# Kernel optimization log

Measured on AMD Instinct MI355X. Metric: run time of the kernel, lower is better.

## Reference

```python
import jax, jax.numpy as jnp
import numpy as np


def setup_inputs() -> dict:
    key = jax.random.key(0)
    k1, k2, k3 = jax.random.split(key, 3)
    N, C_in, H, W = 32, 16, 256, 256
    C_out, K = 64, 3
    x = jax.random.normal(k1, (N, C_in, H, W), dtype=jnp.float32)
    # match nn.Conv2d default init scale roughly (values irrelevant for correctness harness)
    fan_in = C_in * K * K
    bound = 1.0 / np.sqrt(fan_in)
    conv_weight = jax.random.normal(k2, (C_out, C_in, K, K), dtype=jnp.float32) * bound
    conv_bias = jax.random.normal(k3, (C_out,), dtype=jnp.float32) * bound
    return {"x": x, "conv_weight": conv_weight, "conv_bias": conv_bias}


def reference(x, conv_weight, conv_bias):
    # Conv2d: stride=1, padding=0 (VALID), dilation=1, groups=1
    y = jax.lax.conv_general_dilated(
        x, conv_weight,
        window_strides=(1, 1), padding='VALID',
        dimension_numbers=('NCHW', 'OIHW', 'NCHW'),
    ) + conv_bias[None, :, None, None]          # (N, C_out, OH, OW)
    y = jnp.min(y, axis=1, keepdims=True)       # min over output channels -> (N, 1, OH, OW)
    return jnp.tanh(jnp.tanh(y))                # double tanh
```

## Files before the change

### kernel.cpp

```cpp
#include <hip/hip_runtime.h>
#include <hip/hip_bf16.h>

typedef __attribute__((ext_vector_type(8)))  short short8;
typedef __attribute__((ext_vector_type(4)))  float f32x4;
typedef __attribute__((ext_vector_type(16))) float f32x16;

#define CIN   16
#define HH    256
#define WW    256
#define OHH   254
#define OWW   254
#define HW    (HH * WW)

#define SLOTU  (36 * 8)
#define HALF_R (16 * SLOTU + 8)

__device__ __forceinline__ ushort f2bf(float f) {
    unsigned u = __builtin_bit_cast(unsigned, f);
    unsigned r = (u + 0x7fffu + ((u >> 16) & 1u)) >> 16;
    return (ushort)r;
}

__device__ __forceinline__ float dtanh2(float x) {
    const float K = 2.8853900817779268f;
    float xc = fminf(fmaxf(x, -9.0f), 9.0f);
    float e1 = __builtin_amdgcn_exp2f(K * xc);
    float t1 = 1.0f - 2.0f * __builtin_amdgcn_rcpf(e1 + 1.0f);
    float e2 = __builtin_amdgcn_exp2f(K * t1);
    return 1.0f - 2.0f * __builtin_amdgcn_rcpf(e2 + 1.0f);
}

__global__ void prep_weights(const float* __restrict__ wsrc, ushort* __restrict__ wfrag) {
    int idx = blockIdx.x * 256 + threadIdx.x;
    if (idx >= 9216) return;
    int r    = idx & 7;
    int lane = (idx >> 3) & 63;
    int j    = (idx >> 9) & 1;
    int tap  = idx >> 10;
    int ci   = 8 * (lane >> 5) + r;
    int co   = j * 32 + (lane & 31);
    int kh   = tap / 3, kw = tap - 3 * kh;
    wfrag[idx] = f2bf(wsrc[(co * CIN + ci) * 9 + kh * 3 + kw]);
}

__global__ __launch_bounds__(256, 2) void conv_min_tanh(
        const float* __restrict__ x, const ushort* __restrict__ wfrag,
        const float* __restrict__ bias, float* __restrict__ out) {
    __shared__ ushort ring[2 * HALF_R];
    __shared__ ushort mp[2][2][4][32];

    const int tid   = threadIdx.x;
    const int ow0   = blockIdx.x * 32;
    const int hbase = blockIdx.y * 128;
    const int n     = blockIdx.z;
    const float* xb = x + (size_t)n * CIN * HW;

    auto stage_inline = [&](int pos) {
        int lr  = pos / 36;
        int rm  = pos - lr * 36;
        int ciq = rm / 9;
        int w4  = rm - ciq * 9;
        int hg  = min(hbase + lr, HH - 1);
        int wg  = min(ow0 + 4 * w4, WW - 4);
        const float* src = xb + (size_t)(ciq * 4) * HW + hg * WW + wg;
        f32x4 v0 = *reinterpret_cast<const f32x4*>(src);
        f32x4 v1 = *reinterpret_cast<const f32x4*>(src + HW);
        f32x4 v2 = *reinterpret_cast<const f32x4*>(src + 2 * HW);
        f32x4 v3 = *reinterpret_cast<const f32x4*>(src + 3 * HW);
        ushort* dst = &ring[(ciq >> 1) * HALF_R + lr * SLOTU + (4 * w4) * 8 + (ciq & 1) * 4];
#pragma unroll
        for (int e = 0; e < 4; ++e) {
            unsigned lo, hi;
            asm("v_cvt_pk_bf16_f32 %0, %1, %2" : "=v"(lo) : "v"(v0[e]), "v"(v1[e]));
            asm("v_cvt_pk_bf16_f32 %0, %1, %2" : "=v"(hi) : "v"(v2[e]), "v"(v3[e]));
            uint2 pk; pk.x = lo; pk.y = hi;
            *reinterpret_cast<uint2*>(dst + e * 8) = pk;
        }
    };
    stage_inline(tid);
    if (tid < 32) stage_inline(tid + 256);

    const bool sa = (tid < 144);
    const int lr  = tid / 36;
    const int rm  = tid - lr * 36;
    const int ciq = rm / 9;
    const int w4  = rm - ciq * 9;
    const int wg  = min(ow0 + 4 * w4, WW - 4);
    const float* gbase = xb + (size_t)(ciq * 4) * HW + wg;
    ushort* sdst = &ring[(ciq >> 1) * HALF_R + (4 * w4) * 8 + (ciq & 1) * 4];

    f32x4 ra0 = {}, ra1 = {}, ra2 = {}, ra3 = {};
    f32x4 rb0 = {}, rb1 = {}, rb2 = {}, rb3 = {};

#define ISSUE(cc, r0, r1, r2, r3)                                              \
    if (sa) {                                                                  \
        int hg = min(hbase + 4 * (cc) + lr, HH - 1);                           \
        const float* s_ = gbase + hg * WW;                                     \
        asm volatile("global_load_dwordx4 %0, %1, off" : "=v"(r0) : "v"(s_) : "memory");           \
        asm volatile("global_load_dwordx4 %0, %1, off" : "=v"(r1) : "v"(s_ + HW) : "memory");      \
        asm volatile("global_load_dwordx4 %0, %1, off" : "=v"(r2) : "v"(s_ + 2 * HW) : "memory");  \
        asm volatile("global_load_dwordx4 %0, %1, off" : "=v"(r3) : "v"(s_ + 3 * HW) : "memory");  \
    }

#define WRITEBK(cc, r0, r1, r2, r3)                                            \
    if (sa) {                                                                  \
        ushort* d_ = sdst + ((4 * (cc) + lr) & 15) * SLOTU;                    \
        _Pragma("unroll")                                                      \
        for (int e = 0; e < 4; ++e) {                                          \
            unsigned lo_, hi_;                                                 \
            asm("v_cvt_pk_bf16_f32 %0, %1, %2" : "=v"(lo_) : "v"(r0[e]), "v"(r1[e]));  \
            asm("v_cvt_pk_bf16_f32 %0, %1, %2" : "=v"(hi_) : "v"(r2[e]), "v"(r3[e]));  \
            uint2 pk_; pk_.x = lo_; pk_.y = hi_;                               \
            *reinterpret_cast<uint2*>(d_ + e * 8) = pk_;                       \
        }                                                                      \
    }

    ISSUE(2, ra0, ra1, ra2, ra3);
    ISSUE(3, rb0, rb1, rb2, rb3);

    const int lane  = tid & 63;
    const int wid   = tid >> 6;
    const int jw    = wid & 1;
    const int rq    = wid >> 1;
    const int px    = lane & 31;
    const int khalf = lane >> 5;
    short8 wf[9];
#pragma unroll
    for (int tap = 0; tap < 9; ++tap)
        wf[tap] = *reinterpret_cast<const short8*>(wfrag + ((tap * 2 + jw) * 64 + lane) * 8);
    f32x16 bi;
#pragma unroll
    for (int q4 = 0; q4 < 4; ++q4) {
        f32x4 b = *reinterpret_cast<const f32x4*>(bias + jw * 32 + 4 * khalf + 8 * q4);
#pragma unroll
        for (int s = 0; s < 4; ++s) bi[q4 * 4 + s] = b[s];
    }
    const ushort* bptr = &ring[khalf * HALF_R + px * 8];

    asm volatile("s_waitcnt lgkmcnt(0)" ::: "memory");
    __builtin_amdgcn_s_barrier();

#pragma unroll 2
    for (int c = 0; c < 32; ++c) {
#pragma unroll
        for (int jj = 0; jj < 2; ++jj) {
            const int R = 4 * c + 2 * rq + jj;
            f32x16 a = bi;
#pragma unroll
            for (int kh = 0; kh < 3; ++kh) {
                const ushort* rp = bptr + ((R + kh) & 15) * SLOTU;
#pragma unroll
                for (int kw = 0; kw < 3; ++kw) {
                    short8 b = *reinterpret_cast<const short8*>(rp + kw * 8);
                    a = __builtin_amdgcn_mfma_f32_32x32x16_bf16(wf[kh * 3 + kw], b, a, 0, 0, 0);
                }
            }
            float v = a[0];
#pragma unroll
            for (int r = 1; r < 16; ++r) v = fminf(v, a[r]);
            v = fminf(v, __shfl_xor(v, 32, 64));
            if (lane < 32) mp[c & 1][jw][2 * rq + jj][px] = f2bf(v);
        }

        if (c < 31) {
            if ((c & 1) == 0) {
                asm volatile("s_waitcnt vmcnt(4)"
                             : "+v"(ra0), "+v"(ra1), "+v"(ra2), "+v"(ra3) :: "memory");
                WRITEBK(c + 2, ra0, ra1, ra2, ra3);
                ISSUE(min(c + 4, 32), ra0, ra1, ra2, ra3);
            } else {
                asm volatile("s_waitcnt vmcnt(4)"
                             : "+v"(rb0), "+v"(rb1), "+v"(rb2), "+v"(rb3) :: "memory");
                WRITEBK(c + 2, rb0, rb1, rb2, rb3);
                ISSUE(min(c + 4, 32), rb0, rb1, rb2, rb3);
            }
        }

        asm volatile("s_waitcnt lgkmcnt(0)" ::: "memory");
        __builtin_amdgcn_s_barrier();

        if (tid < 128) {
            const int r4 = tid >> 5, opx = tid & 31;
            float f0 = __builtin_bit_cast(float, (unsigned)mp[c & 1][0][r4][opx] << 16);
            float f1 = __builtin_bit_cast(float, (unsigned)mp[c & 1][1][r4][opx] << 16);
            float y  = dtanh2(fminf(f0, f1));
            const int oh = hbase + 4 * c + r4;
            const int ow = ow0 + opx;
            if (oh < OHH && ow < OWW)
                out[((size_t)n * OHH + oh) * OWW + ow] = y;
        }
    }
#undef ISSUE
#undef WRITEBK
}

extern "C" void kernel_launch(void* const* d_in, const int* in_sizes, int n_in,
                              void* d_out, int out_size, void* d_ws, size_t ws_size,
                              hipStream_t stream) {
    const float* x = (const float*)d_in[0];
    const float* w = (const float*)d_in[1];
    const float* b = (const float*)d_in[2];
    float* out     = (float*)d_out;
    ushort* wfrag  = (ushort*)d_ws;

    prep_weights<<<36, 256, 0, stream>>>(w, wfrag);
    dim3 grid(8, 2, 32);
    conv_min_tanh<<<grid, dim3(256, 1, 1), 0, stream>>>(x, wfrag, b, out);
}
```

Before: 51.85 us.

## Share input row fragments across two output rows and split H into more blocks

Each wave now computes two adjacent output rows at once, loading each of the four input rows' B fragments a single time and feeding them to both accumulators. This removes redundant LDS reads that came from the overlapping 3x3 window rows. The grid is doubled along H, with 64 rows per block, and launch bounds raised to 3 blocks per CU to increase parallelism. The trade-off is more accumulator registers, a longer pipeline prologue relative to each block's work, and a tree-shaped min reduction.

```diff
diff --git a/kernel.cpp b/kernel.cpp
--- a/kernel.cpp
+++ b/kernel.cpp
@@ -28,6 +28,14 @@
     float t1 = 1.0f - 2.0f * __builtin_amdgcn_rcpf(e1 + 1.0f);
     float e2 = __builtin_amdgcn_exp2f(K * t1);
     return 1.0f - 2.0f * __builtin_amdgcn_rcpf(e2 + 1.0f);
+}
+
+__device__ __forceinline__ float rmin16(f32x16 a) {
+    float t0 = fminf(fminf(a[0],  a[1]),  fminf(a[2],  a[3]));
+    float t1 = fminf(fminf(a[4],  a[5]),  fminf(a[6],  a[7]));
+    float t2 = fminf(fminf(a[8],  a[9]),  fminf(a[10], a[11]));
+    float t3 = fminf(fminf(a[12], a[13]), fminf(a[14], a[15]));
+    return fminf(fminf(t0, t1), fminf(t2, t3));
 }
 
 __global__ void prep_weights(const float* __restrict__ wsrc, ushort* __restrict__ wfrag) {
@@ -43,7 +51,7 @@
     wfrag[idx] = f2bf(wsrc[(co * CIN + ci) * 9 + kh * 3 + kw]);
 }
 
-__global__ __launch_bounds__(256, 2) void conv_min_tanh(
+__global__ __launch_bounds__(256, 3) void conv_min_tanh(
         const float* __restrict__ x, const ushort* __restrict__ wfrag,
         const float* __restrict__ bias, float* __restrict__ out) {
     __shared__ ushort ring[2 * HALF_R];
@@ -51,23 +59,23 @@
 
     const int tid   = threadIdx.x;
     const int ow0   = blockIdx.x * 32;
-    const int hbase = blockIdx.y * 128;
+    const int hbase = blockIdx.y * 64;
     const int n     = blockIdx.z;
     const float* xb = x + (size_t)n * CIN * HW;
 
     auto stage_inline = [&](int pos) {
-        int lr  = pos / 36;
-        int rm  = pos - lr * 36;
-        int ciq = rm / 9;
-        int w4  = rm - ciq * 9;
-        int hg  = min(hbase + lr, HH - 1);
-        int wg  = min(ow0 + 4 * w4, WW - 4);
-        const float* src = xb + (size_t)(ciq * 4) * HW + hg * WW + wg;
+        int lr_  = pos / 36;
+        int rm_  = pos - lr_ * 36;
+        int ciq_ = rm_ / 9;
+        int w4_  = rm_ - ciq_ * 9;
+        int hg  = min(hbase + lr_, HH - 1);
+        int wg_ = min(ow0 + 4 * w4_, WW - 4);
+        const float* src = xb + (size_t)(ciq_ * 4) * HW + hg * WW + wg_;
         f32x4 v0 = *reinterpret_cast<const f32x4*>(src);
         f32x4 v1 = *reinterpret_cast<const f32x4*>(src + HW);
         f32x4 v2 = *reinterpret_cast<const f32x4*>(src + 2 * HW);
         f32x4 v3 = *reinterpret_cast<const f32x4*>(src + 3 * HW);
-        ushort* dst = &ring[(ciq >> 1) * HALF_R + lr * SLOTU + (4 * w4) * 8 + (ciq & 1) * 4];
+        ushort* dst = &ring[(ciq_ >> 1) * HALF_R + lr_ * SLOTU + (4 * w4_) * 8 + (ciq_ & 1) * 4];
 #pragma unroll
         for (int e = 0; e < 4; ++e) {
             unsigned lo, hi;
@@ -141,38 +149,47 @@
     __builtin_amdgcn_s_barrier();
 
 #pragma unroll 2
-    for (int c = 0; c < 32; ++c) {
-#pragma unroll
-        for (int jj = 0; jj < 2; ++jj) {
-            const int R = 4 * c + 2 * rq + jj;
-            f32x16 a = bi;
-#pragma unroll
-            for (int kh = 0; kh < 3; ++kh) {
-                const ushort* rp = bptr + ((R + kh) & 15) * SLOTU;
-#pragma unroll
-                for (int kw = 0; kw < 3; ++kw) {
-                    short8 b = *reinterpret_cast<const short8*>(rp + kw * 8);
-                    a = __builtin_amdgcn_mfma_f32_32x32x16_bf16(wf[kh * 3 + kw], b, a, 0, 0, 0);
+    for (int c = 0; c < 16; ++c) {
+        {
+            const int R0 = 4 * c + 2 * rq;
+            f32x16 a0 = bi, a1 = bi;
+#pragma unroll
+            for (int t = 0; t < 4; ++t) {
+                const ushort* rp = bptr + ((R0 + t) & 15) * SLOTU;
+                short8 f0 = *reinterpret_cast<const short8*>(rp);
+                short8 f1 = *reinterpret_cast<const short8*>(rp + 8);
+                short8 f2 = *reinterpret_cast<const short8*>(rp + 16);
+                if (t < 3) {
+                    a0 = __builtin_amdgcn_mfma_f32_32x32x16_bf16(wf[t * 3 + 0], f0, a0, 0, 0, 0);
+                    a0 = __builtin_amdgcn_mfma_f32_32x32x16_bf16(wf[t * 3 + 1], f1, a0, 0, 0, 0);
+                    a0 = __builtin_amdgcn_mfma_f32_32x32x16_bf16(wf[t * 3 + 2], f2, a0, 0, 0, 0);
+                }
+                if (t >= 1) {
+                    a1 = __builtin_amdgcn_mfma_f32_32x32x16_bf16(wf[(t - 1) * 3 + 0], f0, a1, 0, 0, 0);
+                    a1 = __builtin_amdgcn_mfma_f32_32x32x16_bf16(wf[(t - 1) * 3 + 1], f1, a1, 0, 0, 0);
+                    a1 = __builtin_amdgcn_mfma_f32_32x32x16_bf16(wf[(t - 1) * 3 + 2], f2, a1, 0, 0, 0);
                 }
             }
-            float v = a[0];
-#pragma unroll
-            for (int r = 1; r < 16; ++r) v = fminf(v, a[r]);
-            v = fminf(v, __shfl_xor(v, 32, 64));
-            if (lane < 32) mp[c & 1][jw][2 * rq + jj][px] = f2bf(v);
-        }
-
-        if (c < 31) {
+            float v0 = rmin16(a0), v1 = rmin16(a1);
+            v0 = fminf(v0, __shfl_xor(v0, 32, 64));
+            v1 = fminf(v1, __shfl_xor(v1, 32, 64));
+            if (lane < 32) {
+                mp[c & 1][jw][2 * rq + 0][px] = f2bf(v0);
+                mp[c & 1][jw][2 * rq + 1][px] = f2bf(v1);
+            }
+        }
+
+        if (c < 15) {
             if ((c & 1) == 0) {
                 asm volatile("s_waitcnt vmcnt(4)"
                              : "+v"(ra0), "+v"(ra1), "+v"(ra2), "+v"(ra3) :: "memory");
                 WRITEBK(c + 2, ra0, ra1, ra2, ra3);
-                ISSUE(min(c + 4, 32), ra0, ra1, ra2, ra3);
+                ISSUE(min(c + 4, 16), ra0, ra1, ra2, ra3);
             } else {
                 asm volatile("s_waitcnt vmcnt(4)"
                              : "+v"(rb0), "+v"(rb1), "+v"(rb2), "+v"(rb3) :: "memory");
                 WRITEBK(c + 2, rb0, rb1, rb2, rb3);
-                ISSUE(min(c + 4, 32), rb0, rb1, rb2, rb3);
+                ISSUE(min(c + 4, 16), rb0, rb1, rb2, rb3);
             }
         }
 
@@ -204,6 +221,6 @@
     ushort* wfrag  = (ushort*)d_ws;
 
     prep_weights<<<36, 256, 0, stream>>>(w, wfrag);
-    dim3 grid(8, 2, 32);
+    dim3 grid(8, 4, 32);
     conv_min_tanh<<<grid, dim3(256, 1, 1), 0, stream>>>(x, wfrag, b, out);
 }
```

Measured after the change: 56.18 us. 1.08x slower.
